# Kernel tuning notes

Hardware: AMD Instinct MI355X
Metric: run time of the kernel (lower is better)

Reference implementation:

```python
import jax, jax.numpy as jnp
import numpy as np

HIDDEN = 2048
HEADS = 16
HEAD_DIM = HIDDEN // HEADS  # 128


def setup_inputs() -> dict:
    key = jax.random.key(0)
    ks = jax.random.split(key, 9)
    B, S = 2, 2048
    x = jax.random.normal(ks[0], (B, S, HIDDEN), dtype=jnp.float32)
    scale = 1.0 / np.sqrt(HIDDEN)
    Wq = jax.random.normal(ks[1], (HIDDEN, HIDDEN), dtype=jnp.float32) * scale
    Wk = jax.random.normal(ks[2], (HIDDEN, HIDDEN), dtype=jnp.float32) * scale
    Wv = jax.random.normal(ks[3], (HIDDEN, HIDDEN), dtype=jnp.float32) * scale
    Wo = jax.random.normal(ks[4], (HIDDEN, HIDDEN), dtype=jnp.float32) * scale
    bq = jnp.zeros((HIDDEN,), dtype=jnp.float32)
    bk = jnp.zeros((HIDDEN,), dtype=jnp.float32)
    bv = jnp.zeros((HIDDEN,), dtype=jnp.float32)
    bo = jnp.zeros((HIDDEN,), dtype=jnp.float32)
    return {"x": x, "Wq": Wq, "bq": bq, "Wk": Wk, "bk": bk,
            "Wv": Wv, "bv": bv, "Wo": Wo, "bo": bo}


def reference(x, Wq, bq, Wk, bk, Wv, bv, Wo, bo):
    B, S, H = x.shape
    nh, hd = HEADS, HEAD_DIM
    # projections: Linear stores W as [out, in], applies x @ W.T + b
    q = (x @ Wq.T + bq).reshape(B, S, nh, hd).transpose(0, 2, 1, 3)  # [B,nh,S,hd]
    k = (x @ Wk.T + bk).reshape(B, S, nh, hd).transpose(0, 2, 1, 3)
    v = (x @ Wv.T + bv).reshape(B, S, nh, hd).transpose(0, 2, 1, 3)
    scores = jnp.einsum("bhqd,bhkd->bhqk", q, k) / np.sqrt(hd)  # [B,nh,S,S]
    causal = jnp.tril(jnp.ones((S, S), dtype=bool))
    scores = jnp.where(causal[None, None], scores, -jnp.inf)
    probs = jax.nn.softmax(scores, axis=-1)
    attn = jnp.einsum("bhqk,bhkd->bhqd", probs, v)  # [B,nh,S,hd]
    y = attn.transpose(0, 2, 1, 3).reshape(B, S, H)
    return y @ Wo.T + bo
```

## Files before the change

### kernel.cpp

```cpp
#include <hip/hip_runtime.h>

#define HIDDEN 2048
#define NH 16
#define HD 128
#define BATCH 2
#define SEQ 2048

typedef __attribute__((ext_vector_type(8))) short short8;
typedef __attribute__((ext_vector_type(4))) float floatx4;

__device__ inline unsigned short f2bf(float f) {
  union { float f; unsigned int u; } x; x.f = f;
  unsigned int r = x.u + 0x7fffu + ((x.u >> 16) & 1u);
  return (unsigned short)(r >> 16);
}
__device__ inline unsigned int pkbf(float a, float b) {
  return (unsigned int)f2bf(a) | ((unsigned int)f2bf(b) << 16);
}

__device__ inline void async_cp16(const void* g, void* l) {
  __builtin_amdgcn_global_load_lds(
      (const __attribute__((address_space(1))) unsigned int*)g,
      (__attribute__((address_space(3))) unsigned int*)l, 16, 0, 0);
}

__global__ __launch_bounds__(256) void cvt_kernel(const float* __restrict__ in,
                                                  unsigned short* __restrict__ out,
                                                  int n) {
  int i = (blockIdx.x * 256 + threadIdx.x) * 4;
  if (i + 3 < n) {
    float4 v = *reinterpret_cast<const float4*>(in + i);
    ushort4 o;
    o.x = f2bf(v.x); o.y = f2bf(v.y); o.z = f2bf(v.z); o.w = f2bf(v.w);
    *reinterpret_cast<ushort4*>(out + i) = o;
  }
}

struct QkvPtrs {
  const unsigned short* W[3];
  const float* b[3];
  unsigned short* oq[3];
  float oscale[3];
};

template<int MODE>
__global__ __launch_bounds__(512, 2) void gemm_nt(const unsigned short* __restrict__ A,
                                                  QkvPtrs P,
                                                  float* __restrict__ outF) {
  __shared__ __align__(16) unsigned short As[3][16384];
  __shared__ __align__(16) unsigned short Bs[3][8192];
  const int t = threadIdx.x;
  const int lane = t & 63;
  const int w = t >> 6;
  const int wr = w >> 1, wc = w & 1;
  const int g = lane >> 4;
  const int l15 = lane & 15;

  const int nwg = gridDim.x;
  int bid = blockIdx.x;
  int Wi = (bid & 7) * (nwg >> 3) + (bid >> 3);
  const int bx = Wi & 15;
  const int byy = Wi >> 4;
  const int wsel = (MODE == 0) ? (byy >> 4) : 0;
  const int row0 = bx * 256;
  const int col0 = (MODE == 0) ? ((byy & 15) * 128) : (byy * 128);

  const unsigned short* Bw = P.W[wsel];
  const float* bias = P.b[wsel];

  floatx4 acc[4][4] = {};

#define STAGE(KT, BUF)                                                              \
  {                                                                                 \
    const int kb_ = (KT) * 64;                                                      \
    _Pragma("unroll")                                                               \
    for (int i_ = 0; i_ < 4; ++i_) {                                                \
      int c_ = t + i_ * 512;                                                        \
      async_cp16(A + (size_t)(row0 + (c_ & 255)) * 2048 + kb_ + (c_ >> 8) * 8,      \
                 &As[BUF][c_ * 8]);                                                 \
    }                                                                               \
    _Pragma("unroll")                                                               \
    for (int i_ = 0; i_ < 2; ++i_) {                                                \
      int c_ = t + i_ * 512;                                                        \
      async_cp16(Bw + (size_t)(col0 + (c_ & 127)) * 2048 + kb_ + (c_ >> 7) * 8,     \
                 &Bs[BUF][c_ * 8]);                                                 \
    }                                                                               \
  }

  STAGE(0, 0);
  STAGE(1, 1);
  asm volatile("s_waitcnt vmcnt(6)" ::: "memory");
  __builtin_amdgcn_s_barrier();
  __builtin_amdgcn_sched_barrier(0);

  int cb = 0;
  for (int kt = 0; kt < 32; ++kt) {
    const bool pf = (kt + 2 < 32);
    if (pf) {
      const int nb = (cb + 2 >= 3) ? (cb - 1) : (cb + 2);
      STAGE(kt + 2, nb);
    }
    short8 af[2][4], bf[2][4];
#pragma unroll
    for (int ks = 0; ks < 2; ++ks) {
#pragma unroll
      for (int m = 0; m < 4; ++m)
        af[ks][m] = *(const short8*)
            &As[cb][((ks * 4 + g) * 256 + wr * 64 + m * 16 + l15) * 8];
#pragma unroll
      for (int n = 0; n < 4; ++n)
        bf[ks][n] = *(const short8*)
            &Bs[cb][((ks * 4 + g) * 128 + wc * 64 + n * 16 + l15) * 8];
    }
    __builtin_amdgcn_s_setprio(1);
#pragma unroll
    for (int ks = 0; ks < 2; ++ks)
#pragma unroll
      for (int m = 0; m < 4; ++m)
#pragma unroll
        for (int n = 0; n < 4; ++n)
          acc[m][n] = __builtin_amdgcn_mfma_f32_16x16x32_bf16(af[ks][m], bf[ks][n],
                                                              acc[m][n], 0, 0, 0);
    __builtin_amdgcn_s_setprio(0);
    if (pf)
      asm volatile("s_waitcnt vmcnt(6)" ::: "memory");
    else
      asm volatile("s_waitcnt vmcnt(0)" ::: "memory");
    __builtin_amdgcn_s_barrier();
    __builtin_amdgcn_sched_barrier(0);
    cb = (cb + 1 >= 3) ? 0 : (cb + 1);
  }
#undef STAGE

  const float osc = P.oscale[wsel];
#pragma unroll
  for (int m = 0; m < 4; ++m) {
#pragma unroll
    for (int n = 0; n < 4; ++n) {
      int gcol = col0 + wc * 64 + n * 16 + l15;
      float bv = bias[gcol];
#pragma unroll
      for (int r = 0; r < 4; ++r) {
        int grow = row0 + wr * 64 + m * 16 + g * 4 + r;
        float v = acc[m][n][r] + bv;
        if (MODE == 1) {
          outF[(size_t)grow * 2048 + gcol] = v;
        } else {
          int bb = grow >> 11;
          int ss = grow & 2047;
          int hh = gcol >> 7;
          int dd = gcol & 127;
          P.oq[wsel][(((size_t)bb * NH + hh) * SEQ + ss) * HD + dd] = f2bf(v * osc);
        }
      }
    }
  }
}

__global__ __launch_bounds__(256) void attn_kernel(const unsigned short* __restrict__ Q,
                                                   const unsigned short* __restrict__ Kg,
                                                   const unsigned short* __restrict__ Vg,
                                                   unsigned short* __restrict__ O) {
  __shared__ __align__(16) unsigned short Ks[16 * 64 * 8];
  __shared__ __align__(16) unsigned short VT[8 * 128 * 8];

  const int t = threadIdx.x;
  const int lane = t & 63;
  const int w = t >> 6;
  const int g = lane >> 4;
  const int l15 = lane & 15;

  int gid = blockIdx.x;
  int Wi = (gid < 256) ? gid : 767 - gid;
  const int bx = Wi & 15;
  const int bh = Wi >> 4;
  const int q0 = bx * 128;
  const int bb = bh >> 4;
  const int hh = bh & 15;

  const unsigned short* Qb = Q + (size_t)bh * SEQ * HD;
  const unsigned short* Kb = Kg + (size_t)bh * SEQ * HD;
  const unsigned short* Vb = Vg + (size_t)bh * SEQ * HD;

  const int qw = q0 + w * 32;

  short8 bq[2][4];
#pragma unroll
  for (int qh = 0; qh < 2; ++qh)
#pragma unroll
    for (int kb = 0; kb < 4; ++kb)
      bq[qh][kb] = *(const short8*)(Qb + (size_t)(qw + qh * 16 + l15) * HD + kb * 32 + g * 8);

  floatx4 acc[2][8] = {};
  float mrun[2] = {-1e30f, -1e30f};
  float lrun[2] = {0.f, 0.f};

  const int ntiles = (q0 >> 6) + 2;
  for (int tk = 0; tk < ntiles; ++tk) {
    const int k0 = tk * 64;
    __syncthreads();
#pragma unroll
    for (int cc = 0; cc < 4; ++cc) {
      int c = t + cc * 256;
      int k8 = c >> 6, s = c & 63;
      int kvs = ((s >> 5) << 5) + (((s >> 2) & 3) << 3) + (((s >> 4) & 1) << 2) + (s & 3);
      async_cp16(Kb + (size_t)(k0 + kvs) * HD + k8 * 8, &Ks[c * 8]);
    }
#pragma unroll
    for (int cc = 0; cc < 2; ++cc) {
      int c = t + cc * 256;
      int kv = (c >> 4) * 2;
      int d0 = (c & 15) * 8;
      int row = kv >> 3;
      short8 va = *(const short8*)(Vb + (size_t)(k0 + kv) * HD + d0);
      short8 vb = *(const short8*)(Vb + (size_t)(k0 + kv + 1) * HD + d0);
#pragma unroll
      for (int j = 0; j < 8; ++j) {
        int d = d0 + j;
        int dp = d ^ (((d >> 3) ^ row) & 7);
        unsigned int u = (unsigned short)va[j] | ((unsigned int)(unsigned short)vb[j] << 16);
        *(unsigned int*)&VT[(row * 128 + dp) * 8 + (kv & 7)] = u;
      }
    }
    __syncthreads();

    floatx4 sv[4][2];
#pragma unroll
    for (int kvh = 0; kvh < 4; ++kvh) {
      sv[kvh][0] = (floatx4){0.f, 0.f, 0.f, 0.f};
      sv[kvh][1] = (floatx4){0.f, 0.f, 0.f, 0.f};
#pragma unroll
      for (int kb = 0; kb < 4; ++kb) {
        short8 ak = *(const short8*)&Ks[((kb * 4 + g) * 64 + kvh * 16 + l15) * 8];
        sv[kvh][0] = __builtin_amdgcn_mfma_f32_16x16x32_bf16(ak, bq[0][kb], sv[kvh][0], 0, 0, 0);
        sv[kvh][1] = __builtin_amdgcn_mfma_f32_16x16x32_bf16(ak, bq[1][kb], sv[kvh][1], 0, 0, 0);
      }
    }

    if (k0 + 63 > qw) {
#pragma unroll
      for (int kvh = 0; kvh < 4; ++kvh)
#pragma unroll
        for (int qh = 0; qh < 2; ++qh)
#pragma unroll
          for (int r = 0; r < 4; ++r) {
            int kvg = k0 + ((kvh >> 1) << 5) + g * 8 + ((kvh & 1) << 2) + r;
            int qg = qw + qh * 16 + l15;
            if (kvg > qg) sv[kvh][qh][r] = -1e30f;
          }
    }

#pragma unroll
    for (int qh = 0; qh < 2; ++qh) {
      float mt = sv[0][qh][0];
#pragma unroll
      for (int kvh = 0; kvh < 4; ++kvh)
#pragma unroll
        for (int r = 0; r < 4; ++r)
          mt = fmaxf(mt, sv[kvh][qh][r]);
      mt = fmaxf(mt, __shfl_xor(mt, 16, 64));
      mt = fmaxf(mt, __shfl_xor(mt, 32, 64));
      float mnew = fmaxf(mrun[qh], mt);
      float f = __expf(mrun[qh] - mnew);
      mrun[qh] = mnew;
      float ssum = 0.f;
#pragma unroll
      for (int kvh = 0; kvh < 4; ++kvh)
#pragma unroll
        for (int r = 0; r < 4; ++r) {
          float p = __expf(sv[kvh][qh][r] - mnew);
          sv[kvh][qh][r] = p;
          ssum += p;
        }
      ssum += __shfl_xor(ssum, 16, 64);
      ssum += __shfl_xor(ssum, 32, 64);
      lrun[qh] = lrun[qh] * f + ssum;
      float fr[4];
#pragma unroll
      for (int r = 0; r < 4; ++r)
        fr[r] = __shfl(f, (lane & 48) + 4 * g + r, 64);
#pragma unroll
      for (int db = 0; db < 8; ++db)
#pragma unroll
        for (int r = 0; r < 4; ++r)
          acc[qh][db][r] *= fr[r];
    }

#pragma unroll
    for (int kh = 0; kh < 2; ++kh) {
      union { short8 s8; unsigned int u[4]; } p0, p1;
      p0.u[0] = pkbf(sv[2 * kh][0][0], sv[2 * kh][0][1]);
      p0.u[1] = pkbf(sv[2 * kh][0][2], sv[2 * kh][0][3]);
      p0.u[2] = pkbf(sv[2 * kh + 1][0][0], sv[2 * kh + 1][0][1]);
      p0.u[3] = pkbf(sv[2 * kh + 1][0][2], sv[2 * kh + 1][0][3]);
      p1.u[0] = pkbf(sv[2 * kh][1][0], sv[2 * kh][1][1]);
      p1.u[1] = pkbf(sv[2 * kh][1][2], sv[2 * kh][1][3]);
      p1.u[2] = pkbf(sv[2 * kh + 1][1][0], sv[2 * kh + 1][1][1]);
      p1.u[3] = pkbf(sv[2 * kh + 1][1][2], sv[2 * kh + 1][1][3]);
      int row = kh * 4 + g;
#pragma unroll
      for (int db = 0; db < 8; ++db) {
        int d = db * 16 + l15;
        int dp = d ^ (((d >> 3) ^ row) & 7);
        short8 bv = *(const short8*)&VT[(row * 128 + dp) * 8];
        acc[0][db] = __builtin_amdgcn_mfma_f32_16x16x32_bf16(p0.s8, bv, acc[0][db], 0, 0, 0);
        acc[1][db] = __builtin_amdgcn_mfma_f32_16x16x32_bf16(p1.s8, bv, acc[1][db], 0, 0, 0);
      }
    }
  }

#pragma unroll
  for (int qh = 0; qh < 2; ++qh) {
    float inv = 1.0f / lrun[qh];
    float ir[4];
#pragma unroll
    for (int r = 0; r < 4; ++r)
      ir[r] = __shfl(inv, (lane & 48) + 4 * g + r, 64);
#pragma unroll
    for (int r = 0; r < 4; ++r) {
      int qg = qw + qh * 16 + 4 * g + r;
      size_t base = ((size_t)bb * SEQ + qg) * HIDDEN + hh * HD;
#pragma unroll
      for (int db = 0; db < 8; ++db)
        O[base + db * 16 + l15] = f2bf(acc[qh][db][r] * ir[r]);
    }
  }
}

extern "C" void kernel_launch(void* const* d_in, const int* in_sizes, int n_in,
                              void* d_out, int out_size, void* d_ws, size_t ws_size,
                              hipStream_t stream) {
  (void)in_sizes; (void)n_in; (void)out_size;
  const float* x  = (const float*)d_in[0];
  const float* Wq = (const float*)d_in[1];
  const float* bq = (const float*)d_in[2];
  const float* Wk = (const float*)d_in[3];
  const float* bk = (const float*)d_in[4];
  const float* Wv = (const float*)d_in[5];
  const float* bv = (const float*)d_in[6];
  const float* Wo = (const float*)d_in[7];
  const float* bo = (const float*)d_in[8];
  float* out = (float*)d_out;

  const float qscale = 0.08838834764831845f;
  char* ws = (char*)d_ws;
  dim3 blk(256);
  dim3 gblk(512);
  const bool fused = ws_size >= 92274688ull;

  if (fused) {
    unsigned short* xbf = (unsigned short*)ws;
    unsigned short* W0  = (unsigned short*)(ws + 16777216);
    unsigned short* W1  = (unsigned short*)(ws + 25165824);
    unsigned short* W2  = (unsigned short*)(ws + 33554432);
    unsigned short* Qbf = (unsigned short*)(ws + 41943040);
    unsigned short* Kbf = (unsigned short*)(ws + 58720256);
    unsigned short* Vbf = (unsigned short*)(ws + 75497472);

    cvt_kernel<<<8192, blk, 0, stream>>>(x, xbf, BATCH * SEQ * HIDDEN);
    cvt_kernel<<<4096, blk, 0, stream>>>(Wq, W0, HIDDEN * HIDDEN);
    cvt_kernel<<<4096, blk, 0, stream>>>(Wk, W1, HIDDEN * HIDDEN);
    cvt_kernel<<<4096, blk, 0, stream>>>(Wv, W2, HIDDEN * HIDDEN);

    QkvPtrs Pq;
    Pq.W[0] = W0;  Pq.W[1] = W1;  Pq.W[2] = W2;
    Pq.b[0] = bq;  Pq.b[1] = bk;  Pq.b[2] = bv;
    Pq.oq[0] = Qbf; Pq.oq[1] = Kbf; Pq.oq[2] = Vbf;
    Pq.oscale[0] = qscale; Pq.oscale[1] = 1.0f; Pq.oscale[2] = 1.0f;
    gemm_nt<0><<<768, gblk, 0, stream>>>(xbf, Pq, nullptr);

    attn_kernel<<<512, blk, 0, stream>>>(Qbf, Kbf, Vbf, xbf);

    cvt_kernel<<<4096, blk, 0, stream>>>(Wo, W0, HIDDEN * HIDDEN);
    QkvPtrs Po;
    Po.W[0] = W0; Po.W[1] = W0; Po.W[2] = W0;
    Po.b[0] = bo; Po.b[1] = bo; Po.b[2] = bo;
    Po.oq[0] = nullptr; Po.oq[1] = nullptr; Po.oq[2] = nullptr;
    Po.oscale[0] = 1.0f; Po.oscale[1] = 1.0f; Po.oscale[2] = 1.0f;
    gemm_nt<1><<<256, gblk, 0, stream>>>(xbf, Po, out);
  } else {
    unsigned short* xbf = (unsigned short*)ws;
    unsigned short* Wbf = (unsigned short*)(ws + 16777216);
    unsigned short* Qbf = (unsigned short*)(ws + 25165824);
    unsigned short* Kbf = (unsigned short*)(ws + 41943040);
    unsigned short* Vbf = (unsigned short*)(ws + 58720256);

    cvt_kernel<<<8192, blk, 0, stream>>>(x, xbf, BATCH * SEQ * HIDDEN);

    const float* biases[3] = {bq, bk, bv};
    const float* wsrc[3] = {Wq, Wk, Wv};
    unsigned short* outs[3] = {Qbf, Kbf, Vbf};
    float oscales[3] = {qscale, 1.0f, 1.0f};
    for (int i = 0; i < 3; ++i) {
      cvt_kernel<<<4096, blk, 0, stream>>>(wsrc[i], Wbf, HIDDEN * HIDDEN);
      QkvPtrs Pp;
      Pp.W[0] = Wbf; Pp.W[1] = Wbf; Pp.W[2] = Wbf;
      Pp.b[0] = biases[i]; Pp.b[1] = biases[i]; Pp.b[2] = biases[i];
      Pp.oq[0] = outs[i]; Pp.oq[1] = outs[i]; Pp.oq[2] = outs[i];
      Pp.oscale[0] = oscales[i]; Pp.oscale[1] = oscales[i]; Pp.oscale[2] = oscales[i];
      gemm_nt<0><<<256, gblk, 0, stream>>>(xbf, Pp, nullptr);
    }

    attn_kernel<<<512, blk, 0, stream>>>(Qbf, Kbf, Vbf, xbf);

    cvt_kernel<<<4096, blk, 0, stream>>>(Wo, Wbf, HIDDEN * HIDDEN);
    QkvPtrs Po;
    Po.W[0] = Wbf; Po.W[1] = Wbf; Po.W[2] = Wbf;
    Po.b[0] = bo; Po.b[1] = bo; Po.b[2] = bo;
    Po.oq[0] = nullptr; Po.oq[1] = nullptr; Po.oq[2] = nullptr;
    Po.oscale[0] = 1.0f; Po.oscale[1] = 1.0f; Po.oscale[2] = 1.0f;
    gemm_nt<1><<<256, gblk, 0, stream>>>(xbf, Po, out);
  }
}
```

Baseline: 624.7 us.

## Shrink GEMM tiles to 128x128 with single-buffered LDS and 256 threads

Replaces the 256x128-tile, 512-thread GEMM with a triple-buffered async pipeline by a 128x128-tile, 256-thread kernel. It uses one LDS buffer, a K step of 32, and two barriers per iteration. The launch grids double to match the smaller tiles. This cuts LDS use per block and raises block count, possibly allowing more occupancy, but removes load/compute overlap and lowers data reuse per tile.

```diff
diff --git a/kernel.cpp b/kernel.cpp
--- a/kernel.cpp
+++ b/kernel.cpp
@@ -44,11 +44,11 @@
 };
 
 template<int MODE>
-__global__ __launch_bounds__(512, 2) void gemm_nt(const unsigned short* __restrict__ A,
-                                                  QkvPtrs P,
-                                                  float* __restrict__ outF) {
-  __shared__ __align__(16) unsigned short As[3][16384];
-  __shared__ __align__(16) unsigned short Bs[3][8192];
+__global__ __launch_bounds__(256) void gemm_nt(const unsigned short* __restrict__ A,
+                                               QkvPtrs P,
+                                               float* __restrict__ outF) {
+  __shared__ __align__(16) unsigned short As[4096];
+  __shared__ __align__(16) unsigned short Bs[4096];
   const int t = threadIdx.x;
   const int lane = t & 63;
   const int w = t >> 6;
@@ -59,10 +59,10 @@
   const int nwg = gridDim.x;
   int bid = blockIdx.x;
   int Wi = (bid & 7) * (nwg >> 3) + (bid >> 3);
-  const int bx = Wi & 15;
-  const int byy = Wi >> 4;
+  const int bx = Wi & 31;
+  const int byy = Wi >> 5;
   const int wsel = (MODE == 0) ? (byy >> 4) : 0;
-  const int row0 = bx * 256;
+  const int row0 = bx * 128;
   const int col0 = (MODE == 0) ? ((byy & 15) * 128) : (byy * 128);
 
   const unsigned short* Bw = P.W[wsel];
@@ -70,65 +70,37 @@
 
   floatx4 acc[4][4] = {};
 
-#define STAGE(KT, BUF)                                                              \
-  {                                                                                 \
-    const int kb_ = (KT) * 64;                                                      \
-    _Pragma("unroll")                                                               \
-    for (int i_ = 0; i_ < 4; ++i_) {                                                \
-      int c_ = t + i_ * 512;                                                        \
-      async_cp16(A + (size_t)(row0 + (c_ & 255)) * 2048 + kb_ + (c_ >> 8) * 8,      \
-                 &As[BUF][c_ * 8]);                                                 \
-    }                                                                               \
-    _Pragma("unroll")                                                               \
-    for (int i_ = 0; i_ < 2; ++i_) {                                                \
-      int c_ = t + i_ * 512;                                                        \
-      async_cp16(Bw + (size_t)(col0 + (c_ & 127)) * 2048 + kb_ + (c_ >> 7) * 8,     \
-                 &Bs[BUF][c_ * 8]);                                                 \
-    }                                                                               \
-  }
-
-  STAGE(0, 0);
-  STAGE(1, 1);
-  asm volatile("s_waitcnt vmcnt(6)" ::: "memory");
-  __builtin_amdgcn_s_barrier();
-  __builtin_amdgcn_sched_barrier(0);
-
-  int cb = 0;
-  for (int kt = 0; kt < 32; ++kt) {
-    const bool pf = (kt + 2 < 32);
-    if (pf) {
-      const int nb = (cb + 2 >= 3) ? (cb - 1) : (cb + 2);
-      STAGE(kt + 2, nb);
-    }
-    short8 af[2][4], bf[2][4];
-#pragma unroll
-    for (int ks = 0; ks < 2; ++ks) {
-#pragma unroll
-      for (int m = 0; m < 4; ++m)
-        af[ks][m] = *(const short8*)
-            &As[cb][((ks * 4 + g) * 256 + wr * 64 + m * 16 + l15) * 8];
+#define STAGE(KT)                                                               \
+  {                                                                             \
+    const int kb_ = (KT) * 32;                                                  \
+    _Pragma("unroll")                                                           \
+    for (int cc_ = 0; cc_ < 2; ++cc_) {                                         \
+      int c_ = t + cc_ * 256;                                                   \
+      int k8_ = c_ >> 7, r_ = c_ & 127;                                         \
+      async_cp16(A + (size_t)(row0 + r_) * 2048 + kb_ + k8_ * 8, &As[c_ * 8]);  \
+      async_cp16(Bw + (size_t)(col0 + r_) * 2048 + kb_ + k8_ * 8, &Bs[c_ * 8]); \
+    }                                                                           \
+  }
+
+  STAGE(0);
+  for (int kt = 0; kt < 64; ++kt) {
+    __syncthreads();
+    short8 af[4], bf[4];
+#pragma unroll
+    for (int m = 0; m < 4; ++m)
+      af[m] = *(const short8*)&As[(g * 128 + wr * 64 + m * 16 + l15) * 8];
+#pragma unroll
+    for (int n = 0; n < 4; ++n)
+      bf[n] = *(const short8*)&Bs[(g * 128 + wc * 64 + n * 16 + l15) * 8];
+#pragma unroll
+    for (int m = 0; m < 4; ++m)
 #pragma unroll
       for (int n = 0; n < 4; ++n)
-        bf[ks][n] = *(const short8*)
-            &Bs[cb][((ks * 4 + g) * 128 + wc * 64 + n * 16 + l15) * 8];
-    }
-    __builtin_amdgcn_s_setprio(1);
-#pragma unroll
-    for (int ks = 0; ks < 2; ++ks)
-#pragma unroll
-      for (int m = 0; m < 4; ++m)
-#pragma unroll
-        for (int n = 0; n < 4; ++n)
-          acc[m][n] = __builtin_amdgcn_mfma_f32_16x16x32_bf16(af[ks][m], bf[ks][n],
-                                                              acc[m][n], 0, 0, 0);
-    __builtin_amdgcn_s_setprio(0);
-    if (pf)
-      asm volatile("s_waitcnt vmcnt(6)" ::: "memory");
-    else
-      asm volatile("s_waitcnt vmcnt(0)" ::: "memory");
-    __builtin_amdgcn_s_barrier();
-    __builtin_amdgcn_sched_barrier(0);
-    cb = (cb + 1 >= 3) ? 0 : (cb + 1);
+        acc[m][n] = __builtin_amdgcn_mfma_f32_16x16x32_bf16(af[m], bf[n], acc[m][n], 0, 0, 0);
+    if (kt < 63) {
+      __syncthreads();
+      STAGE(kt + 1);
+    }
   }
 #undef STAGE
 
@@ -345,7 +317,6 @@
   const float qscale = 0.08838834764831845f;
   char* ws = (char*)d_ws;
   dim3 blk(256);
-  dim3 gblk(512);
   const bool fused = ws_size >= 92274688ull;
 
   if (fused) {
@@ -367,7 +338,7 @@
     Pq.b[0] = bq;  Pq.b[1] = bk;  Pq.b[2] = bv;
     Pq.oq[0] = Qbf; Pq.oq[1] = Kbf; Pq.oq[2] = Vbf;
     Pq.oscale[0] = qscale; Pq.oscale[1] = 1.0f; Pq.oscale[2] = 1.0f;
-    gemm_nt<0><<<768, gblk, 0, stream>>>(xbf, Pq, nullptr);
+    gemm_nt<0><<<1536, blk, 0, stream>>>(xbf, Pq, nullptr);
 
     attn_kernel<<<512, blk, 0, stream>>>(Qbf, Kbf, Vbf, xbf);
 
@@ -377,7 +348,7 @@
     Po.b[0] = bo; Po.b[1] = bo; Po.b[2] = bo;
     Po.oq[0] = nullptr; Po.oq[1] = nullptr; Po.oq[2] = nullptr;
     Po.oscale[0] = 1.0f; Po.oscale[1] = 1.0f; Po.oscale[2] = 1.0f;
-    gemm_nt<1><<<256, gblk, 0, stream>>>(xbf, Po, out);
+    gemm_nt<1><<<512, blk, 0, stream>>>(xbf, Po, out);
   } else {
     unsigned short* xbf = (unsigned short*)ws;
     unsigned short* Wbf = (unsigned short*)(ws + 16777216);
@@ -398,7 +369,7 @@
       Pp.b[0] = biases[i]; Pp.b[1] = biases[i]; Pp.b[2] = biases[i];
       Pp.oq[0] = outs[i]; Pp.oq[1] = outs[i]; Pp.oq[2] = outs[i];
       Pp.oscale[0] = oscales[i]; Pp.oscale[1] = oscales[i]; Pp.oscale[2] = oscales[i];
-      gemm_nt<0><<<256, gblk, 0, stream>>>(xbf, Pp, nullptr);
+      gemm_nt<0><<<512, blk, 0, stream>>>(xbf, Pp, nullptr);
     }
 
     attn_kernel<<<512, blk, 0, stream>>>(Qbf, Kbf, Vbf, xbf);
@@ -409,6 +380,6 @@
     Po.b[0] = bo; Po.b[1] = bo; Po.b[2] = bo;
     Po.oq[0] = nullptr; Po.oq[1] = nullptr; Po.oq[2] = nullptr;
     Po.oscale[0] = 1.0f; Po.oscale[1] = 1.0f; Po.oscale[2] = 1.0f;
-    gemm_nt<1><<<256, gblk, 0, stream>>>(xbf, Po, out);
-  }
-}
+    gemm_nt<1><<<512, blk, 0, stream>>>(xbf, Po, out);
+  }
+}
```

Measured after the change: 603.8 us. 1.03x faster.

## Interleave GEMM LDS reads, async prefetch and MFMA in four barrier-synced phases

Applied to the files above, without the earlier changes.

Splits each k-tile of the projection GEMM into four phases. Each phase reads a slice of A/B fragments from LDS, issues part of the next tile's global-to-LDS prefetch, then runs eight MFMAs, with block barriers and setprio around each phase. Source pointers are precomputed once, and the launch-bounds hint of 2 blocks per CU is dropped. The aim is to overlap LDS reads and global loads with matrix-core work and to cut per-iteration address arithmetic. The cost is many more barriers per iteration and a possible change in register allocation.

```diff
diff --git a/kernel.cpp b/kernel.cpp
--- a/kernel.cpp
+++ b/kernel.cpp
@@ -44,9 +44,9 @@
 };
 
 template<int MODE>
-__global__ __launch_bounds__(512, 2) void gemm_nt(const unsigned short* __restrict__ A,
-                                                  QkvPtrs P,
-                                                  float* __restrict__ outF) {
+__global__ __launch_bounds__(512) void gemm_nt(const unsigned short* __restrict__ A,
+                                               QkvPtrs P,
+                                               float* __restrict__ outF) {
   __shared__ __align__(16) unsigned short As[3][16384];
   __shared__ __align__(16) unsigned short Bs[3][8192];
   const int t = threadIdx.x;
@@ -68,27 +68,32 @@
   const unsigned short* Bw = P.W[wsel];
   const float* bias = P.b[wsel];
 
+  const unsigned short* srcA[4];
+  const unsigned short* srcB[2];
+  int dstA[4], dstB[2];
+#pragma unroll
+  for (int i = 0; i < 4; ++i) {
+    int c = t + i * 512;
+    srcA[i] = A + (size_t)(row0 + (c & 255)) * 2048 + (c >> 8) * 8;
+    dstA[i] = c * 8;
+  }
+#pragma unroll
+  for (int i = 0; i < 2; ++i) {
+    int c = t + i * 512;
+    srcB[i] = Bw + (size_t)(col0 + (c & 127)) * 2048 + (c >> 7) * 8;
+    dstB[i] = c * 8;
+  }
+
   floatx4 acc[4][4] = {};
 
-#define STAGE(KT, BUF)                                                              \
-  {                                                                                 \
-    const int kb_ = (KT) * 64;                                                      \
-    _Pragma("unroll")                                                               \
-    for (int i_ = 0; i_ < 4; ++i_) {                                                \
-      int c_ = t + i_ * 512;                                                        \
-      async_cp16(A + (size_t)(row0 + (c_ & 255)) * 2048 + kb_ + (c_ >> 8) * 8,      \
-                 &As[BUF][c_ * 8]);                                                 \
-    }                                                                               \
-    _Pragma("unroll")                                                               \
-    for (int i_ = 0; i_ < 2; ++i_) {                                                \
-      int c_ = t + i_ * 512;                                                        \
-      async_cp16(Bw + (size_t)(col0 + (c_ & 127)) * 2048 + kb_ + (c_ >> 7) * 8,     \
-                 &Bs[BUF][c_ * 8]);                                                 \
-    }                                                                               \
-  }
-
-  STAGE(0, 0);
-  STAGE(1, 1);
+#pragma unroll
+  for (int i = 0; i < 4; ++i) async_cp16(srcA[i], &As[0][dstA[i]]);
+#pragma unroll
+  for (int i = 0; i < 2; ++i) async_cp16(srcB[i], &Bs[0][dstB[i]]);
+#pragma unroll
+  for (int i = 0; i < 4; ++i) async_cp16(srcA[i] + 64, &As[1][dstA[i]]);
+#pragma unroll
+  for (int i = 0; i < 2; ++i) async_cp16(srcB[i] + 64, &Bs[1][dstB[i]]);
   asm volatile("s_waitcnt vmcnt(6)" ::: "memory");
   __builtin_amdgcn_s_barrier();
   __builtin_amdgcn_sched_barrier(0);
@@ -96,31 +101,81 @@
   int cb = 0;
   for (int kt = 0; kt < 32; ++kt) {
     const bool pf = (kt + 2 < 32);
-    if (pf) {
-      const int nb = (cb + 2 >= 3) ? (cb - 1) : (cb + 2);
-      STAGE(kt + 2, nb);
-    }
-    short8 af[2][4], bf[2][4];
-#pragma unroll
-    for (int ks = 0; ks < 2; ++ks) {
-#pragma unroll
-      for (int m = 0; m < 4; ++m)
-        af[ks][m] = *(const short8*)
-            &As[cb][((ks * 4 + g) * 256 + wr * 64 + m * 16 + l15) * 8];
+    const int nb = (cb + 2 >= 3) ? (cb - 1) : (cb + 2);
+    const int kbn = (kt + 2) * 64;
+    const unsigned short* a0 = &As[cb][0];
+    const unsigned short* b0 = &Bs[cb][0];
+
+    short8 bfr[2][4], af[2];
+
+#pragma unroll
+    for (int n = 0; n < 4; ++n)
+      bfr[0][n] = *(const short8*)&b0[((0 * 4 + g) * 128 + wc * 64 + n * 16 + l15) * 8];
+    af[0] = *(const short8*)&a0[((0 * 4 + g) * 256 + wr * 64 + 0 * 16 + l15) * 8];
+    af[1] = *(const short8*)&a0[((0 * 4 + g) * 256 + wr * 64 + 1 * 16 + l15) * 8];
+    if (pf) { async_cp16(srcA[0] + kbn, &As[nb][dstA[0]]);
+              async_cp16(srcA[1] + kbn, &As[nb][dstA[1]]); }
+    __builtin_amdgcn_s_barrier();
+    asm volatile("s_waitcnt lgkmcnt(0)" ::: "memory");
+    __builtin_amdgcn_sched_barrier(0);
+    __builtin_amdgcn_s_setprio(1);
+#pragma unroll
+    for (int m = 0; m < 2; ++m)
 #pragma unroll
       for (int n = 0; n < 4; ++n)
-        bf[ks][n] = *(const short8*)
-            &Bs[cb][((ks * 4 + g) * 128 + wc * 64 + n * 16 + l15) * 8];
-    }
+        acc[m][n] = __builtin_amdgcn_mfma_f32_16x16x32_bf16(af[m], bfr[0][n], acc[m][n], 0, 0, 0);
+    __builtin_amdgcn_s_setprio(0);
+    __builtin_amdgcn_s_barrier();
+    __builtin_amdgcn_sched_barrier(0);
+
+#pragma unroll
+    for (int n = 0; n < 4; ++n)
+      bfr[1][n] = *(const short8*)&b0[((1 * 4 + g) * 128 + wc * 64 + n * 16 + l15) * 8];
+    af[0] = *(const short8*)&a0[((1 * 4 + g) * 256 + wr * 64 + 0 * 16 + l15) * 8];
+    af[1] = *(const short8*)&a0[((1 * 4 + g) * 256 + wr * 64 + 1 * 16 + l15) * 8];
+    if (pf) { async_cp16(srcA[2] + kbn, &As[nb][dstA[2]]);
+              async_cp16(srcA[3] + kbn, &As[nb][dstA[3]]); }
+    __builtin_amdgcn_s_barrier();
+    asm volatile("s_waitcnt lgkmcnt(0)" ::: "memory");
+    __builtin_amdgcn_sched_barrier(0);
     __builtin_amdgcn_s_setprio(1);
 #pragma unroll
-    for (int ks = 0; ks < 2; ++ks)
-#pragma unroll
-      for (int m = 0; m < 4; ++m)
-#pragma unroll
-        for (int n = 0; n < 4; ++n)
-          acc[m][n] = __builtin_amdgcn_mfma_f32_16x16x32_bf16(af[ks][m], bf[ks][n],
-                                                              acc[m][n], 0, 0, 0);
+    for (int m = 0; m < 2; ++m)
+#pragma unroll
+      for (int n = 0; n < 4; ++n)
+        acc[m][n] = __builtin_amdgcn_mfma_f32_16x16x32_bf16(af[m], bfr[1][n], acc[m][n], 0, 0, 0);
+    __builtin_amdgcn_s_setprio(0);
+    __builtin_amdgcn_s_barrier();
+    __builtin_amdgcn_sched_barrier(0);
+
+    af[0] = *(const short8*)&a0[((0 * 4 + g) * 256 + wr * 64 + 2 * 16 + l15) * 8];
+    af[1] = *(const short8*)&a0[((0 * 4 + g) * 256 + wr * 64 + 3 * 16 + l15) * 8];
+    if (pf) { async_cp16(srcB[0] + kbn, &Bs[nb][dstB[0]]);
+              async_cp16(srcB[1] + kbn, &Bs[nb][dstB[1]]); }
+    __builtin_amdgcn_s_barrier();
+    asm volatile("s_waitcnt lgkmcnt(0)" ::: "memory");
+    __builtin_amdgcn_sched_barrier(0);
+    __builtin_amdgcn_s_setprio(1);
+#pragma unroll
+    for (int m = 0; m < 2; ++m)
+#pragma unroll
+      for (int n = 0; n < 4; ++n)
+        acc[m + 2][n] = __builtin_amdgcn_mfma_f32_16x16x32_bf16(af[m], bfr[0][n], acc[m + 2][n], 0, 0, 0);
+    __builtin_amdgcn_s_setprio(0);
+    __builtin_amdgcn_s_barrier();
+    __builtin_amdgcn_sched_barrier(0);
+
+    af[0] = *(const short8*)&a0[((1 * 4 + g) * 256 + wr * 64 + 2 * 16 + l15) * 8];
+    af[1] = *(const short8*)&a0[((1 * 4 + g) * 256 + wr * 64 + 3 * 16 + l15) * 8];
+    __builtin_amdgcn_s_barrier();
+    asm volatile("s_waitcnt lgkmcnt(0)" ::: "memory");
+    __builtin_amdgcn_sched_barrier(0);
+    __builtin_amdgcn_s_setprio(1);
+#pragma unroll
+    for (int m = 0; m < 2; ++m)
+#pragma unroll
+      for (int n = 0; n < 4; ++n)
+        acc[m + 2][n] = __builtin_amdgcn_mfma_f32_16x16x32_bf16(af[m], bfr[1][n], acc[m + 2][n], 0, 0, 0);
     __builtin_amdgcn_s_setprio(0);
     if (pf)
       asm volatile("s_waitcnt vmcnt(6)" ::: "memory");
@@ -128,9 +183,9 @@
       asm volatile("s_waitcnt vmcnt(0)" ::: "memory");
     __builtin_amdgcn_s_barrier();
     __builtin_amdgcn_sched_barrier(0);
+
     cb = (cb + 1 >= 3) ? 0 : (cb + 1);
   }
-#undef STAGE
 
   const float osc = P.oscale[wsel];
 #pragma unroll
```

Measured after the change: 537.4 us. 14.0% less time.

## Halve GEMM K-tile for higher occupancy and merge fp32-to-bf16 conversions

Applied to the files above, without the earlier changes.

The GEMM K-tile shrinks from 64 to 32, which halves shared memory per block, and launch bounds now ask for 4 blocks per CU instead of 2. Prefetch addresses are precomputed, and the LDS fragment reads are issued before the next async stage. A single cvt_all launch now converts x and all four weights when the workspace is large enough, replacing five separate conversion kernels. This cuts launch overhead and targets better latency hiding, at the cost of twice as many barriers per K-loop and more register pressure under the tighter launch bound.

```diff
diff --git a/kernel.cpp b/kernel.cpp
--- a/kernel.cpp
+++ b/kernel.cpp
@@ -36,6 +36,22 @@
   }
 }
 
+struct CvtAll {
+  const float* src[5];
+  unsigned short* dst[5];
+};
+__global__ __launch_bounds__(256) void cvt_all(CvtAll C) {
+  int b = blockIdx.x;
+  int r, off;
+  if (b < 8192) { r = 0; off = b; }
+  else { int q = b - 8192; r = 1 + (q >> 12); off = q & 4095; }
+  int i = (off * 256 + threadIdx.x) * 4;
+  float4 v = *reinterpret_cast<const float4*>(C.src[r] + i);
+  ushort4 o;
+  o.x = f2bf(v.x); o.y = f2bf(v.y); o.z = f2bf(v.z); o.w = f2bf(v.w);
+  *reinterpret_cast<ushort4*>(C.dst[r] + i) = o;
+}
+
 struct QkvPtrs {
   const unsigned short* W[3];
   const float* b[3];
@@ -44,11 +60,11 @@
 };
 
 template<int MODE>
-__global__ __launch_bounds__(512, 2) void gemm_nt(const unsigned short* __restrict__ A,
+__global__ __launch_bounds__(512, 4) void gemm_nt(const unsigned short* __restrict__ A,
                                                   QkvPtrs P,
                                                   float* __restrict__ outF) {
-  __shared__ __align__(16) unsigned short As[3][16384];
-  __shared__ __align__(16) unsigned short Bs[3][8192];
+  __shared__ __align__(16) unsigned short As[3][8192];
+  __shared__ __align__(16) unsigned short Bs[3][4096];
   const int t = threadIdx.x;
   const int lane = t & 63;
   const int w = t >> 6;
@@ -68,66 +84,58 @@
   const unsigned short* Bw = P.W[wsel];
   const float* bias = P.b[wsel];
 
+  const unsigned short* srcA0 = A + (size_t)(row0 + (t & 255)) * 2048 + (t >> 8) * 8;
+  const unsigned short* srcA1 = A + (size_t)(row0 + ((t + 512) & 255)) * 2048 + ((t + 512) >> 8) * 8;
+  const unsigned short* srcB0 = Bw + (size_t)(col0 + (t & 127)) * 2048 + (t >> 7) * 8;
+  const int dA0 = t * 8, dA1 = (t + 512) * 8, dB0 = t * 8;
+
   floatx4 acc[4][4] = {};
 
-#define STAGE(KT, BUF)                                                              \
-  {                                                                                 \
-    const int kb_ = (KT) * 64;                                                      \
-    _Pragma("unroll")                                                               \
-    for (int i_ = 0; i_ < 4; ++i_) {                                                \
-      int c_ = t + i_ * 512;                                                        \
-      async_cp16(A + (size_t)(row0 + (c_ & 255)) * 2048 + kb_ + (c_ >> 8) * 8,      \
-                 &As[BUF][c_ * 8]);                                                 \
-    }                                                                               \
-    _Pragma("unroll")                                                               \
-    for (int i_ = 0; i_ < 2; ++i_) {                                                \
-      int c_ = t + i_ * 512;                                                        \
-      async_cp16(Bw + (size_t)(col0 + (c_ & 127)) * 2048 + kb_ + (c_ >> 7) * 8,     \
-                 &Bs[BUF][c_ * 8]);                                                 \
-    }                                                                               \
+#define STAGE(KT, BUF)                                   \
+  {                                                      \
+    const int kb_ = (KT) * 32;                           \
+    async_cp16(srcA0 + kb_, &As[BUF][dA0]);              \
+    async_cp16(srcA1 + kb_, &As[BUF][dA1]);              \
+    async_cp16(srcB0 + kb_, &Bs[BUF][dB0]);              \
   }
 
   STAGE(0, 0);
   STAGE(1, 1);
-  asm volatile("s_waitcnt vmcnt(6)" ::: "memory");
+  asm volatile("s_waitcnt vmcnt(3)" ::: "memory");
   __builtin_amdgcn_s_barrier();
   __builtin_amdgcn_sched_barrier(0);
 
   int cb = 0;
-  for (int kt = 0; kt < 32; ++kt) {
-    const bool pf = (kt + 2 < 32);
-    if (pf) {
-      const int nb = (cb + 2 >= 3) ? (cb - 1) : (cb + 2);
-      STAGE(kt + 2, nb);
-    }
-    short8 af[2][4], bf[2][4];
-#pragma unroll
-    for (int ks = 0; ks < 2; ++ks) {
-#pragma unroll
-      for (int m = 0; m < 4; ++m)
-        af[ks][m] = *(const short8*)
-            &As[cb][((ks * 4 + g) * 256 + wr * 64 + m * 16 + l15) * 8];
+  for (int kt = 0; kt < 64; ++kt) {
+    const bool pf = (kt + 2 < 64);
+    const int nb = (cb + 2 >= 3) ? (cb - 1) : (cb + 2);
+
+    short8 af[4], bf[4];
+#pragma unroll
+    for (int m = 0; m < 4; ++m)
+      af[m] = *(const short8*)&As[cb][(g * 256 + wr * 64 + m * 16 + l15) * 8];
+#pragma unroll
+    for (int n = 0; n < 4; ++n)
+      bf[n] = *(const short8*)&Bs[cb][(g * 128 + wc * 64 + n * 16 + l15) * 8];
+    if (pf) STAGE(kt + 2, nb);
+
+    __builtin_amdgcn_s_barrier();
+    asm volatile("s_waitcnt lgkmcnt(0)" ::: "memory");
+    __builtin_amdgcn_sched_barrier(0);
+    __builtin_amdgcn_s_setprio(1);
+#pragma unroll
+    for (int m = 0; m < 4; ++m)
 #pragma unroll
       for (int n = 0; n < 4; ++n)
-        bf[ks][n] = *(const short8*)
-            &Bs[cb][((ks * 4 + g) * 128 + wc * 64 + n * 16 + l15) * 8];
-    }
-    __builtin_amdgcn_s_setprio(1);
-#pragma unroll
-    for (int ks = 0; ks < 2; ++ks)
-#pragma unroll
-      for (int m = 0; m < 4; ++m)
-#pragma unroll
-        for (int n = 0; n < 4; ++n)
-          acc[m][n] = __builtin_amdgcn_mfma_f32_16x16x32_bf16(af[ks][m], bf[ks][n],
-                                                              acc[m][n], 0, 0, 0);
+        acc[m][n] = __builtin_amdgcn_mfma_f32_16x16x32_bf16(af[m], bf[n], acc[m][n], 0, 0, 0);
     __builtin_amdgcn_s_setprio(0);
     if (pf)
-      asm volatile("s_waitcnt vmcnt(6)" ::: "memory");
+      asm volatile("s_waitcnt vmcnt(3)" ::: "memory");
     else
       asm volatile("s_waitcnt vmcnt(0)" ::: "memory");
     __builtin_amdgcn_s_barrier();
     __builtin_amdgcn_sched_barrier(0);
+
     cb = (cb + 1 >= 3) ? 0 : (cb + 1);
   }
 #undef STAGE
@@ -346,9 +354,41 @@
   char* ws = (char*)d_ws;
   dim3 blk(256);
   dim3 gblk(512);
-  const bool fused = ws_size >= 92274688ull;
-
-  if (fused) {
+
+  if (ws_size >= 100663296ull) {
+    unsigned short* xbf = (unsigned short*)ws;
+    unsigned short* W0  = (unsigned short*)(ws + 16777216);
+    unsigned short* W1  = (unsigned short*)(ws + 25165824);
+    unsigned short* W2  = (unsigned short*)(ws + 33554432);
+    unsigned short* W3  = (unsigned short*)(ws + 41943040);
+    unsigned short* Qbf = (unsigned short*)(ws + 50331648);
+    unsigned short* Kbf = (unsigned short*)(ws + 67108864);
+    unsigned short* Vbf = (unsigned short*)(ws + 83886080);
+
+    CvtAll C;
+    C.src[0] = x;   C.dst[0] = xbf;
+    C.src[1] = Wq;  C.dst[1] = W0;
+    C.src[2] = Wk;  C.dst[2] = W1;
+    C.src[3] = Wv;  C.dst[3] = W2;
+    C.src[4] = Wo;  C.dst[4] = W3;
+    cvt_all<<<24576, blk, 0, stream>>>(C);
+
+    QkvPtrs Pq;
+    Pq.W[0] = W0;  Pq.W[1] = W1;  Pq.W[2] = W2;
+    Pq.b[0] = bq;  Pq.b[1] = bk;  Pq.b[2] = bv;
+    Pq.oq[0] = Qbf; Pq.oq[1] = Kbf; Pq.oq[2] = Vbf;
+    Pq.oscale[0] = qscale; Pq.oscale[1] = 1.0f; Pq.oscale[2] = 1.0f;
+    gemm_nt<0><<<768, gblk, 0, stream>>>(xbf, Pq, nullptr);
+
+    attn_kernel<<<512, blk, 0, stream>>>(Qbf, Kbf, Vbf, xbf);
+
+    QkvPtrs Po;
+    Po.W[0] = W3; Po.W[1] = W3; Po.W[2] = W3;
+    Po.b[0] = bo; Po.b[1] = bo; Po.b[2] = bo;
+    Po.oq[0] = nullptr; Po.oq[1] = nullptr; Po.oq[2] = nullptr;
+    Po.oscale[0] = 1.0f; Po.oscale[1] = 1.0f; Po.oscale[2] = 1.0f;
+    gemm_nt<1><<<256, gblk, 0, stream>>>(xbf, Po, out);
+  } else if (ws_size >= 92274688ull) {
     unsigned short* xbf = (unsigned short*)ws;
     unsigned short* W0  = (unsigned short*)(ws + 16777216);
     unsigned short* W1  = (unsigned short*)(ws + 25165824);
@@ -369,9 +409,9 @@
     Pq.oscale[0] = qscale; Pq.oscale[1] = 1.0f; Pq.oscale[2] = 1.0f;
     gemm_nt<0><<<768, gblk, 0, stream>>>(xbf, Pq, nullptr);
 
+    cvt_kernel<<<4096, blk, 0, stream>>>(Wo, W0, HIDDEN * HIDDEN);
     attn_kernel<<<512, blk, 0, stream>>>(Qbf, Kbf, Vbf, xbf);
 
-    cvt_kernel<<<4096, blk, 0, stream>>>(Wo, W0, HIDDEN * HIDDEN);
     QkvPtrs Po;
     Po.W[0] = W0; Po.W[1] = W0; Po.W[2] = W0;
     Po.b[0] = bo; Po.b[1] = bo; Po.b[2] = bo;
```

After: 552.9 us. 11.5% less time.
